# Kernel optimization log

Hardware: AMD Instinct MI355X
Metric: run time of the kernel (lower is better)

## Reference

```python
import jax, jax.numpy as jnp
import numpy as np

EPS = 1e-8

def _l2_normalize(v):
    # torch F.normalize: v / max(||v||_2, eps)
    n = jnp.sqrt(jnp.sum(v * v, axis=1, keepdims=True))
    return v / jnp.maximum(n, EPS)

def setup_inputs() -> dict:
    key = jax.random.key(0)
    k1, k2, k3, k4, k5 = jax.random.split(key, 5)
    B, D, N, C = 1024, 256, 200000, 1000
    x = jax.random.normal(k1, (B, D), dtype=jnp.float32)
    mean = jax.random.normal(k2, (D,), dtype=jnp.float32)
    inv_std = jax.random.uniform(k3, (D,), dtype=jnp.float32)
    train_x = jax.random.normal(k4, (N, D), dtype=jnp.float32)
    train_y = jax.random.randint(k5, (N,), 0, C, dtype=jnp.int64)
    return {"x": x, "mean": mean, "inv_std": inv_std,
            "train_x": train_x, "train_y": train_y}

def reference(x, mean, inv_std, train_x, train_y):
    NUM_CLASSES, K, TEMP = 1000, 20, 20.0
    B = x.shape[0]
    # buffer prep from __init__: normalize train bank rows
    tx = _l2_normalize(train_x)                      # [N, D]
    # forward: standardize + normalize queries
    q = _l2_normalize((x.reshape(B, -1) - mean) * inv_std)  # [B, D]
    sim = q @ tx.T                                   # [B, N]
    k = min(K, tx.shape[0])
    vals, idx = jax.lax.top_k(sim, k)                # [B, k]
    weights = jax.nn.softmax(vals * TEMP, axis=1)    # [B, k]
    labs = train_y[idx]                              # [B, k] gather labels
    out = jnp.zeros((B, NUM_CLASSES), dtype=jnp.float32)
    out = out.at[jnp.arange(B)[:, None], labs].add(weights)
    return out
```

## Files before the change

kernel.cpp:

```cpp
#include <hip/hip_runtime.h>
#include <math.h>

#define BQ     1024
#define D      256
#define NTRAIN 200000
#define CCLS   1000
#define KTOP   20
#define KC     24
#define TEMPF  20.0f
#define EPSV   1e-8f

#define NSEG    64
#define SEGROWS 3125
#define SEGT    49
#define QT      128
#define SSTR    68

typedef __attribute__((ext_vector_type(8))) short bf16x8;
typedef __attribute__((ext_vector_type(4))) float f32x4;

static __device__ __forceinline__ unsigned short f2bf(float f) {
  unsigned int u = __float_as_uint(f);
  u += 0x7FFFu + ((u >> 16) & 1u);
  return (unsigned short)(u >> 16);
}

__global__ void prep_q(const float* __restrict__ x, const float* __restrict__ mean,
                       const float* __restrict__ inv_std,
                       float* __restrict__ qf, unsigned short* __restrict__ qb) {
  int row = blockIdx.x;
  int t = threadIdx.x;
  float v = (x[row * D + t] - mean[t]) * inv_std[t];
  float s = v * v;
  #pragma unroll
  for (int off = 32; off; off >>= 1) s += __shfl_down(s, off);
  __shared__ float red[4];
  if ((t & 63) == 0) red[t >> 6] = s;
  __syncthreads();
  float tot = red[0] + red[1] + red[2] + red[3];
  float scale = 1.0f / fmaxf(sqrtf(tot), EPSV);
  float qv = v * scale;
  qf[row * D + t] = qv;
  qb[row * D + t] = f2bf(qv);
}

__global__ void bank_prep(const float* __restrict__ tx,
                          unsigned short* __restrict__ txb, float* __restrict__ rnorm) {
  int lane = threadIdx.x & 63;
  int row = blockIdx.x * 4 + (threadIdx.x >> 6);
  const float4* p = reinterpret_cast<const float4*>(tx + (size_t)row * D);
  float4 a = p[lane];
  float s = a.x * a.x + a.y * a.y + a.z * a.z + a.w * a.w;
  #pragma unroll
  for (int off = 32; off; off >>= 1) s += __shfl_xor(s, off);
  float rn = 1.0f / fmaxf(sqrtf(s), EPSV);
  if (lane == 0) rnorm[row] = rn;
  ushort4 us;
  us.x = f2bf(a.x * rn); us.y = f2bf(a.y * rn);
  us.z = f2bf(a.z * rn); us.w = f2bf(a.w * rn);
  *reinterpret_cast<ushort4*>(txb + (size_t)row * D + lane * 4) = us;
}

__global__ __launch_bounds__(256, 2)
void knn_mfma(const unsigned short* __restrict__ qb, const unsigned short* __restrict__ txb,
              float* __restrict__ pvals, int* __restrict__ pidx) {
  __shared__ float S[QT * SSTR];

  int t = threadIdx.x;
  int lane = t & 63;
  int w = t >> 6;
  int c = lane & 15, g = lane >> 4;

  int b = blockIdx.x;
  int seg = (b & 7) * 8 + ((b >> 3) & 7);
  int qt  = b >> 6;
  int qbase = qt * QT;
  int wq = qbase + w * 32;

  bf16x8 af[2][8];
  #pragma unroll
  for (int mf = 0; mf < 2; ++mf)
    #pragma unroll
    for (int ks = 0; ks < 8; ++ks)
      af[mf][ks] = *reinterpret_cast<const bf16x8*>(
          qb + (size_t)(wq + mf * 16 + c) * D + ks * 32 + g * 8);

  float tvv[KC]; int tii[KC];
  #pragma unroll
  for (int i = 0; i < KC; ++i) { tvv[i] = -INFINITY; tii[i] = 0; }
  float tmin = -INFINITY;

  auto insert24 = [&](float v, int gi) {
    bool done = false;
    #pragma unroll
    for (int i = 0; i < KC; ++i) {
      bool hit = (!done) && (tvv[i] == tmin);
      if (hit) { tvv[i] = v; tii[i] = gi; done = true; }
    }
    tmin = tvv[0];
    #pragma unroll
    for (int i = 1; i < KC; ++i) tmin = fminf(tmin, tvv[i]);
  };

  int nseg0 = seg * SEGROWS;
  int nsegEnd = nseg0 + SEGROWS;
  int q = t >> 1, pp = t & 1;

  for (int tile = 0; tile < SEGT; ++tile) {
    int nbase = nseg0 + tile * 64;

    f32x4 acc[2][4];
    #pragma unroll
    for (int mf = 0; mf < 2; ++mf)
      #pragma unroll
      for (int nf = 0; nf < 4; ++nf) acc[mf][nf] = (f32x4){0.f, 0.f, 0.f, 0.f};

    #pragma unroll
    for (int ks = 0; ks < 8; ++ks) {
      bf16x8 bfr[4];
      #pragma unroll
      for (int nf = 0; nf < 4; ++nf) {
        int row = nbase + nf * 16 + c;
        row = (row < NTRAIN) ? row : (NTRAIN - 1);
        bfr[nf] = *reinterpret_cast<const bf16x8*>(
            txb + (size_t)row * D + ks * 32 + g * 8);
      }
      #pragma unroll
      for (int nf = 0; nf < 4; ++nf) {
        acc[0][nf] = __builtin_amdgcn_mfma_f32_16x16x32_bf16(af[0][ks], bfr[nf], acc[0][nf], 0, 0, 0);
        acc[1][nf] = __builtin_amdgcn_mfma_f32_16x16x32_bf16(af[1][ks], bfr[nf], acc[1][nf], 0, 0, 0);
      }
    }

    __syncthreads();
    #pragma unroll
    for (int mf = 0; mf < 2; ++mf)
      #pragma unroll
      for (int nf = 0; nf < 4; ++nf)
        #pragma unroll
        for (int r = 0; r < 4; ++r)
          S[(w * 32 + mf * 16 + g * 4 + r) * SSTR + nf * 16 + c] = acc[mf][nf][r];
    __syncthreads();

    #pragma unroll 1
    for (int jj = 0; jj < 8; ++jj) {
      f32x4 v4 = *reinterpret_cast<const f32x4*>(&S[q * SSTR + pp * 32 + jj * 4]);
      int g0 = nbase + pp * 32 + jj * 4;
      #pragma unroll
      for (int e = 0; e < 4; ++e) {
        if (g0 + e < nsegEnd && v4[e] > tmin) insert24(v4[e], g0 + e);
      }
    }
  }

  __syncthreads();
  float* MV = S;
  int*   MI = reinterpret_cast<int*>(S + QT * KC);
  if (pp == 1) {
    #pragma unroll
    for (int i = 0; i < KC; ++i) { MV[q * KC + i] = tvv[i]; MI[q * KC + i] = tii[i]; }
  }
  __syncthreads();
  if (pp == 0) {
    #pragma unroll 1
    for (int i = 0; i < KC; ++i) {
      float v = MV[q * KC + i]; int gi = MI[q * KC + i];
      if (v > tmin) insert24(v, gi);
    }
    int base = ((qbase + q) * NSEG + seg) * KC;
    #pragma unroll
    for (int i = 0; i < KC; ++i) { pvals[base + i] = tvv[i]; pidx[base + i] = tii[i]; }
  }
}

#define NCAND (NSEG * KC)
__global__ void final_sel(const float* __restrict__ pvals, const int* __restrict__ pidx,
                          const float* __restrict__ qf, const float* __restrict__ tx,
                          const float* __restrict__ rnorm, const int* __restrict__ train_y,
                          float* __restrict__ out) {
  __shared__ float cv[NCAND];
  __shared__ int   ci[NCAND];
  __shared__ float qs[D];
  __shared__ float wvv[4 * KC];
  __shared__ int   wii[4 * KC];
  __shared__ float selv[KC];
  __shared__ int   seli[KC];
  __shared__ float rsc[KC];
  __shared__ float ordv[KTOP];
  __shared__ int   ordi[KTOP];
  __shared__ float outrow[CCLS];

  int bq = blockIdx.x;
  int t = threadIdx.x, lane = t & 63, w = t >> 6;

  for (int j = t; j < CCLS; j += 256) outrow[j] = 0.f;
  qs[t] = qf[bq * D + t];
  #pragma unroll
  for (int i = 0; i < 6; ++i) {
    int j = i * 256 + t;
    cv[j] = pvals[(size_t)bq * NCAND + j];
    ci[j] = pidx[(size_t)bq * NCAND + j];
  }
  __syncthreads();

  float lv[6]; int li[6];
  #pragma unroll
  for (int i = 0; i < 6; ++i) { int j = w * 384 + i * 64 + lane; lv[i] = cv[j]; li[i] = ci[j]; }
  for (int it = 0; it < KC; ++it) {
    float bv = -INFINITY; int bi = 0x7fffffff;
    #pragma unroll
    for (int i = 0; i < 6; ++i)
      if (lv[i] > bv || (lv[i] == bv && li[i] < bi)) { bv = lv[i]; bi = li[i]; }
    #pragma unroll
    for (int off = 32; off; off >>= 1) {
      float ov = __shfl_xor(bv, off); int oi = __shfl_xor(bi, off);
      if (ov > bv || (ov == bv && oi < bi)) { bv = ov; bi = oi; }
    }
    #pragma unroll
    for (int i = 0; i < 6; ++i)
      if (li[i] == bi && lv[i] == bv) lv[i] = -INFINITY;
    if (lane == 0) { wvv[w * KC + it] = bv; wii[w * KC + it] = bi; }
  }
  __syncthreads();

  if (w == 0) {
    float m0 = wvv[lane]; int i0 = wii[lane];
    float m1 = (lane < 32) ? wvv[64 + lane] : -INFINITY;
    int   i1 = (lane < 32) ? wii[64 + lane] : 0x7fffffff;
    for (int it = 0; it < KC; ++it) {
      float bv = m0; int bi = i0;
      if (m1 > bv || (m1 == bv && i1 < bi)) { bv = m1; bi = i1; }
      #pragma unroll
      for (int off = 32; off; off >>= 1) {
        float ov = __shfl_xor(bv, off); int oi = __shfl_xor(bi, off);
        if (ov > bv || (ov == bv && oi < bi)) { bv = ov; bi = oi; }
      }
      if (i0 == bi && m0 == bv) m0 = -INFINITY;
      if (i1 == bi && m1 == bv) m1 = -INFINITY;
      if (lane == 0) { selv[it] = bv; seli[it] = bi; }
    }
  }
  __syncthreads();

  for (int k = w; k < KC; k += 4) {
    int idx = seli[k];
    float4 tv = reinterpret_cast<const float4*>(tx + (size_t)idx * D)[lane];
    float4 qv = *reinterpret_cast<const float4*>(&qs[lane * 4]);
    float s = tv.x * qv.x + tv.y * qv.y + tv.z * qv.z + tv.w * qv.w;
    #pragma unroll
    for (int off = 32; off; off >>= 1) s += __shfl_xor(s, off);
    if (lane == 0) rsc[k] = s * rnorm[idx];
  }
  __syncthreads();

  if (w == 0) {
    float v = (lane < KC) ? rsc[lane] : -INFINITY;
    int   i = (lane < KC) ? seli[lane] : 0x7fffffff;
    for (int it = 0; it < KTOP; ++it) {
      float bv = v; int bi = i;
      #pragma unroll
      for (int off = 32; off; off >>= 1) {
        float ov = __shfl_xor(bv, off); int oi = __shfl_xor(bi, off);
        if (ov > bv || (ov == bv && oi < bi)) { bv = ov; bi = oi; }
      }
      if (v == bv && i == bi) v = -INFINITY;
      if (lane == 0) { ordv[it] = bv; ordi[it] = bi; }
    }
    float e = (lane < KTOP) ? expf((ordv[lane] - ordv[0]) * TEMPF) : 0.f;
    float ssum = e;
    #pragma unroll
    for (int off = 32; off; off >>= 1) ssum += __shfl_xor(ssum, off);
    if (lane < KTOP) {
      int label = train_y[ordi[lane]];
      atomicAdd(&outrow[label], e / ssum);
    }
  }
  __syncthreads();
  if (t < 250) reinterpret_cast<float4*>(out)[bq * 250 + t] =
      reinterpret_cast<const float4*>(outrow)[t];
}

extern "C" void kernel_launch(void* const* d_in, const int* in_sizes, int n_in,
                              void* d_out, int out_size, void* d_ws, size_t ws_size,
                              hipStream_t stream) {
  const float* x       = (const float*)d_in[0];
  const float* mean    = (const float*)d_in[1];
  const float* inv_std = (const float*)d_in[2];
  const float* train_x = (const float*)d_in[3];
  const int*   train_y = (const int*)d_in[4];
  float* out = (float*)d_out;

  char* wp = (char*)d_ws;
  float*          qf    = (float*)wp;          wp += (size_t)BQ * D * 4;
  unsigned short* qb    = (unsigned short*)wp; wp += (size_t)BQ * D * 2;
  float*          rnorm = (float*)wp;          wp += (size_t)NTRAIN * 4;
  unsigned short* txb   = (unsigned short*)wp; wp += (size_t)NTRAIN * D * 2;
  float*          pvals = (float*)wp;          wp += (size_t)BQ * NSEG * KC * 4;
  int*            pidx  = (int*)wp;

  prep_q   <<<BQ, 256, 0, stream>>>(x, mean, inv_std, qf, qb);
  bank_prep<<<NTRAIN / 4, 256, 0, stream>>>(train_x, txb, rnorm);
  knn_mfma <<<8 * NSEG, 256, 0, stream>>>(qb, txb, pvals, pidx);
  final_sel<<<BQ, 256, 0, stream>>>(pvals, pidx, qf, train_x, rnorm, train_y, out);
}
```

Measured before the change: 1.459 ms.

## Replace per-thread top-k insertion with two-pass tile-max threshold filtering

The fused GEMM plus register insertion-sort kernel is replaced by three steps. Pass A computes bf16 MFMA similarities and stores only the per-tile maximum for each query. A selection kernel takes the 24th largest tile maximum as a per-query threshold tau. Pass B recomputes the similarities and appends indices scoring at least tau to a capped per-query list using atomics, and the final kernel rescores those candidates in fp32 and picks the top 20. This removes the costly serial insertion logic and LDS round-trips, at the price of running the similarity GEMM twice, extra tmax traffic, and a cap of 256 candidates per query that could overflow.

```diff
diff --git a/kernel.cpp b/kernel.cpp
--- a/kernel.cpp
+++ b/kernel.cpp
@@ -6,15 +6,16 @@
 #define NTRAIN 200000
 #define CCLS   1000
 #define KTOP   20
-#define KC     24
+#define KSEL   24
 #define TEMPF  20.0f
 #define EPSV   1e-8f
 
 #define NSEG    64
 #define SEGROWS 3125
 #define SEGT    49
-#define QT      128
-#define SSTR    68
+#define TGLOB   (NSEG * SEGT)
+#define QTB     64
+#define CAP     256
 
 typedef __attribute__((ext_vector_type(8))) short bf16x8;
 typedef __attribute__((ext_vector_type(4))) float f32x4;
@@ -61,222 +62,214 @@
   *reinterpret_cast<ushort4*>(txb + (size_t)row * D + lane * 4) = us;
 }
 
-__global__ __launch_bounds__(256, 2)
-void knn_mfma(const unsigned short* __restrict__ qb, const unsigned short* __restrict__ txb,
-              float* __restrict__ pvals, int* __restrict__ pidx) {
-  __shared__ float S[QT * SSTR];
-
-  int t = threadIdx.x;
-  int lane = t & 63;
-  int w = t >> 6;
+__global__ __launch_bounds__(256, 4)
+void knn_passA(const unsigned short* __restrict__ qb, const unsigned short* __restrict__ txb,
+               float* __restrict__ tmax) {
+  int t = threadIdx.x, lane = t & 63, w = t >> 6;
   int c = lane & 15, g = lane >> 4;
-
   int b = blockIdx.x;
   int seg = (b & 7) * 8 + ((b >> 3) & 7);
   int qt  = b >> 6;
-  int qbase = qt * QT;
-  int wq = qbase + w * 32;
-
-  bf16x8 af[2][8];
-  #pragma unroll
-  for (int mf = 0; mf < 2; ++mf)
-    #pragma unroll
-    for (int ks = 0; ks < 8; ++ks)
-      af[mf][ks] = *reinterpret_cast<const bf16x8*>(
-          qb + (size_t)(wq + mf * 16 + c) * D + ks * 32 + g * 8);
-
-  float tvv[KC]; int tii[KC];
-  #pragma unroll
-  for (int i = 0; i < KC; ++i) { tvv[i] = -INFINITY; tii[i] = 0; }
-  float tmin = -INFINITY;
-
-  auto insert24 = [&](float v, int gi) {
-    bool done = false;
-    #pragma unroll
-    for (int i = 0; i < KC; ++i) {
-      bool hit = (!done) && (tvv[i] == tmin);
-      if (hit) { tvv[i] = v; tii[i] = gi; done = true; }
-    }
-    tmin = tvv[0];
-    #pragma unroll
-    for (int i = 1; i < KC; ++i) tmin = fminf(tmin, tvv[i]);
-  };
+  int qrow = qt * QTB + w * 16 + c;
+
+  bf16x8 qfr[8];
+  #pragma unroll
+  for (int ks = 0; ks < 8; ++ks)
+    qfr[ks] = *reinterpret_cast<const bf16x8*>(qb + (size_t)qrow * D + ks * 32 + g * 8);
 
   int nseg0 = seg * SEGROWS;
   int nsegEnd = nseg0 + SEGROWS;
-  int q = t >> 1, pp = t & 1;
 
   for (int tile = 0; tile < SEGT; ++tile) {
     int nbase = nseg0 + tile * 64;
-
-    f32x4 acc[2][4];
-    #pragma unroll
-    for (int mf = 0; mf < 2; ++mf)
-      #pragma unroll
-      for (int nf = 0; nf < 4; ++nf) acc[mf][nf] = (f32x4){0.f, 0.f, 0.f, 0.f};
-
+    const unsigned short* tp[4];
+    #pragma unroll
+    for (int nf = 0; nf < 4; ++nf) {
+      int row = nbase + nf * 16 + c;
+      row = (row < nsegEnd) ? row : (nsegEnd - 1);
+      tp[nf] = txb + (size_t)row * D + g * 8;
+    }
+    f32x4 acc[4];
+    #pragma unroll
+    for (int nf = 0; nf < 4; ++nf) acc[nf] = (f32x4){0.f, 0.f, 0.f, 0.f};
     #pragma unroll
     for (int ks = 0; ks < 8; ++ks) {
-      bf16x8 bfr[4];
-      #pragma unroll
-      for (int nf = 0; nf < 4; ++nf) {
-        int row = nbase + nf * 16 + c;
-        row = (row < NTRAIN) ? row : (NTRAIN - 1);
-        bfr[nf] = *reinterpret_cast<const bf16x8*>(
-            txb + (size_t)row * D + ks * 32 + g * 8);
+      bf16x8 tfr[4];
+      #pragma unroll
+      for (int nf = 0; nf < 4; ++nf)
+        tfr[nf] = *reinterpret_cast<const bf16x8*>(tp[nf] + ks * 32);
+      #pragma unroll
+      for (int nf = 0; nf < 4; ++nf)
+        acc[nf] = __builtin_amdgcn_mfma_f32_16x16x32_bf16(tfr[nf], qfr[ks], acc[nf], 0, 0, 0);
+    }
+    float m0 = fmaxf(fmaxf(acc[0][0], acc[0][1]), fmaxf(acc[0][2], acc[0][3]));
+    float m1 = fmaxf(fmaxf(acc[1][0], acc[1][1]), fmaxf(acc[1][2], acc[1][3]));
+    float m2 = fmaxf(fmaxf(acc[2][0], acc[2][1]), fmaxf(acc[2][2], acc[2][3]));
+    float m3 = fmaxf(fmaxf(acc[3][0], acc[3][1]), fmaxf(acc[3][2], acc[3][3]));
+    float mx = fmaxf(fmaxf(m0, m1), fmaxf(m2, m3));
+    mx = fmaxf(mx, __shfl_xor(mx, 16));
+    mx = fmaxf(mx, __shfl_xor(mx, 32));
+    if (g == 0) tmax[(size_t)(seg * SEGT + tile) * BQ + qrow] = mx;
+  }
+}
+
+__global__ void sel_tau(const float* __restrict__ tmax, float* __restrict__ tau) {
+  __shared__ float sv[4]; __shared__ int sj[4];
+  __shared__ float sbv;   __shared__ int sbj;
+  int q = blockIdx.x, t = threadIdx.x, lane = t & 63, w = t >> 6;
+  float v[13];
+  #pragma unroll
+  for (int i = 0; i < 13; ++i) {
+    int jj = i * 256 + t;
+    v[i] = (jj < TGLOB) ? tmax[(size_t)jj * BQ + q] : -INFINITY;
+  }
+  float last = 0.f;
+  for (int it = 0; it < KSEL; ++it) {
+    float bv = -INFINITY; int bj = 0x7fffffff;
+    #pragma unroll
+    for (int i = 0; i < 13; ++i)
+      if (v[i] > bv) { bv = v[i]; bj = i * 256 + t; }
+    #pragma unroll
+    for (int off = 32; off; off >>= 1) {
+      float ov = __shfl_xor(bv, off); int oj = __shfl_xor(bj, off);
+      if (ov > bv || (ov == bv && oj < bj)) { bv = ov; bj = oj; }
+    }
+    if (lane == 0) { sv[w] = bv; sj[w] = bj; }
+    __syncthreads();
+    if (t == 0) {
+      float BV = sv[0]; int BJ = sj[0];
+      #pragma unroll
+      for (int k = 1; k < 4; ++k)
+        if (sv[k] > BV || (sv[k] == BV && sj[k] < BJ)) { BV = sv[k]; BJ = sj[k]; }
+      sbv = BV; sbj = BJ;
+    }
+    __syncthreads();
+    float BV = sbv; int BJ = sbj;
+    #pragma unroll
+    for (int i = 0; i < 13; ++i)
+      if (i * 256 + t == BJ) v[i] = -INFINITY;
+    last = BV;
+    __syncthreads();
+  }
+  if (t == 0) tau[q] = last;
+}
+
+__global__ __launch_bounds__(256, 4)
+void knn_passB(const unsigned short* __restrict__ qb, const unsigned short* __restrict__ txb,
+               const float* __restrict__ tau, int* __restrict__ cnt, int* __restrict__ lists) {
+  int t = threadIdx.x, lane = t & 63, w = t >> 6;
+  int c = lane & 15, g = lane >> 4;
+  int b = blockIdx.x;
+  int seg = (b & 7) * 8 + ((b >> 3) & 7);
+  int qt  = b >> 6;
+  int qrow = qt * QTB + w * 16 + c;
+
+  bf16x8 qfr[8];
+  #pragma unroll
+  for (int ks = 0; ks < 8; ++ks)
+    qfr[ks] = *reinterpret_cast<const bf16x8*>(qb + (size_t)qrow * D + ks * 32 + g * 8);
+  float tq = tau[qrow];
+
+  int nseg0 = seg * SEGROWS;
+  int nsegEnd = nseg0 + SEGROWS;
+
+  for (int tile = 0; tile < SEGT; ++tile) {
+    int nbase = nseg0 + tile * 64;
+    const unsigned short* tp[4];
+    #pragma unroll
+    for (int nf = 0; nf < 4; ++nf) {
+      int row = nbase + nf * 16 + c;
+      row = (row < nsegEnd) ? row : (nsegEnd - 1);
+      tp[nf] = txb + (size_t)row * D + g * 8;
+    }
+    f32x4 acc[4];
+    #pragma unroll
+    for (int nf = 0; nf < 4; ++nf) acc[nf] = (f32x4){0.f, 0.f, 0.f, 0.f};
+    #pragma unroll
+    for (int ks = 0; ks < 8; ++ks) {
+      bf16x8 tfr[4];
+      #pragma unroll
+      for (int nf = 0; nf < 4; ++nf)
+        tfr[nf] = *reinterpret_cast<const bf16x8*>(tp[nf] + ks * 32);
+      #pragma unroll
+      for (int nf = 0; nf < 4; ++nf)
+        acc[nf] = __builtin_amdgcn_mfma_f32_16x16x32_bf16(tfr[nf], qfr[ks], acc[nf], 0, 0, 0);
+    }
+    #pragma unroll
+    for (int nf = 0; nf < 4; ++nf) {
+      #pragma unroll
+      for (int r = 0; r < 4; ++r) {
+        int n = nbase + nf * 16 + g * 4 + r;
+        float v = acc[nf][r];
+        if (n < nsegEnd && v >= tq) {
+          int pos = atomicAdd(&cnt[qrow], 1);
+          if (pos < CAP) lists[(size_t)qrow * CAP + pos] = n;
+        }
       }
-      #pragma unroll
-      for (int nf = 0; nf < 4; ++nf) {
-        acc[0][nf] = __builtin_amdgcn_mfma_f32_16x16x32_bf16(af[0][ks], bfr[nf], acc[0][nf], 0, 0, 0);
-        acc[1][nf] = __builtin_amdgcn_mfma_f32_16x16x32_bf16(af[1][ks], bfr[nf], acc[1][nf], 0, 0, 0);
-      }
-    }
-
-    __syncthreads();
-    #pragma unroll
-    for (int mf = 0; mf < 2; ++mf)
-      #pragma unroll
-      for (int nf = 0; nf < 4; ++nf)
-        #pragma unroll
-        for (int r = 0; r < 4; ++r)
-          S[(w * 32 + mf * 16 + g * 4 + r) * SSTR + nf * 16 + c] = acc[mf][nf][r];
-    __syncthreads();
-
-    #pragma unroll 1
-    for (int jj = 0; jj < 8; ++jj) {
-      f32x4 v4 = *reinterpret_cast<const f32x4*>(&S[q * SSTR + pp * 32 + jj * 4]);
-      int g0 = nbase + pp * 32 + jj * 4;
-      #pragma unroll
-      for (int e = 0; e < 4; ++e) {
-        if (g0 + e < nsegEnd && v4[e] > tmin) insert24(v4[e], g0 + e);
-      }
-    }
-  }
-
-  __syncthreads();
-  float* MV = S;
-  int*   MI = reinterpret_cast<int*>(S + QT * KC);
-  if (pp == 1) {
-    #pragma unroll
-    for (int i = 0; i < KC; ++i) { MV[q * KC + i] = tvv[i]; MI[q * KC + i] = tii[i]; }
-  }
-  __syncthreads();
-  if (pp == 0) {
-    #pragma unroll 1
-    for (int i = 0; i < KC; ++i) {
-      float v = MV[q * KC + i]; int gi = MI[q * KC + i];
-      if (v > tmin) insert24(v, gi);
-    }
-    int base = ((qbase + q) * NSEG + seg) * KC;
-    #pragma unroll
-    for (int i = 0; i < KC; ++i) { pvals[base + i] = tvv[i]; pidx[base + i] = tii[i]; }
-  }
-}
-
-#define NCAND (NSEG * KC)
-__global__ void final_sel(const float* __restrict__ pvals, const int* __restrict__ pidx,
+    }
+  }
+}
+
+__global__ void final_sel(const int* __restrict__ cnt, const int* __restrict__ lists,
                           const float* __restrict__ qf, const float* __restrict__ tx,
                           const float* __restrict__ rnorm, const int* __restrict__ train_y,
                           float* __restrict__ out) {
-  __shared__ float cv[NCAND];
-  __shared__ int   ci[NCAND];
   __shared__ float qs[D];
-  __shared__ float wvv[4 * KC];
-  __shared__ int   wii[4 * KC];
-  __shared__ float selv[KC];
-  __shared__ int   seli[KC];
-  __shared__ float rsc[KC];
-  __shared__ float ordv[KTOP];
-  __shared__ int   ordi[KTOP];
+  __shared__ float rv[CAP]; __shared__ int ri[CAP];
+  __shared__ float sv[4];  __shared__ int sj[4];
+  __shared__ float sbv;    __shared__ int sbj;
+  __shared__ float ordv[KTOP]; __shared__ int ordi[KTOP];
   __shared__ float outrow[CCLS];
-
-  int bq = blockIdx.x;
-  int t = threadIdx.x, lane = t & 63, w = t >> 6;
-
+  int q = blockIdx.x, t = threadIdx.x, lane = t & 63, w = t >> 6;
+
+  qs[t] = qf[q * D + t];
   for (int j = t; j < CCLS; j += 256) outrow[j] = 0.f;
-  qs[t] = qf[bq * D + t];
-  #pragma unroll
-  for (int i = 0; i < 6; ++i) {
-    int j = i * 256 + t;
-    cv[j] = pvals[(size_t)bq * NCAND + j];
-    ci[j] = pidx[(size_t)bq * NCAND + j];
-  }
+  int m = cnt[q]; if (m > CAP) m = CAP;
   __syncthreads();
 
-  float lv[6]; int li[6];
-  #pragma unroll
-  for (int i = 0; i < 6; ++i) { int j = w * 384 + i * 64 + lane; lv[i] = cv[j]; li[i] = ci[j]; }
-  for (int it = 0; it < KC; ++it) {
-    float bv = -INFINITY; int bi = 0x7fffffff;
-    #pragma unroll
-    for (int i = 0; i < 6; ++i)
-      if (lv[i] > bv || (lv[i] == bv && li[i] < bi)) { bv = lv[i]; bi = li[i]; }
-    #pragma unroll
-    for (int off = 32; off; off >>= 1) {
-      float ov = __shfl_xor(bv, off); int oi = __shfl_xor(bi, off);
-      if (ov > bv || (ov == bv && oi < bi)) { bv = ov; bi = oi; }
-    }
-    #pragma unroll
-    for (int i = 0; i < 6; ++i)
-      if (li[i] == bi && lv[i] == bv) lv[i] = -INFINITY;
-    if (lane == 0) { wvv[w * KC + it] = bv; wii[w * KC + it] = bi; }
-  }
-  __syncthreads();
-
-  if (w == 0) {
-    float m0 = wvv[lane]; int i0 = wii[lane];
-    float m1 = (lane < 32) ? wvv[64 + lane] : -INFINITY;
-    int   i1 = (lane < 32) ? wii[64 + lane] : 0x7fffffff;
-    for (int it = 0; it < KC; ++it) {
-      float bv = m0; int bi = i0;
-      if (m1 > bv || (m1 == bv && i1 < bi)) { bv = m1; bi = i1; }
-      #pragma unroll
-      for (int off = 32; off; off >>= 1) {
-        float ov = __shfl_xor(bv, off); int oi = __shfl_xor(bi, off);
-        if (ov > bv || (ov == bv && oi < bi)) { bv = ov; bi = oi; }
-      }
-      if (i0 == bi && m0 == bv) m0 = -INFINITY;
-      if (i1 == bi && m1 == bv) m1 = -INFINITY;
-      if (lane == 0) { selv[it] = bv; seli[it] = bi; }
-    }
-  }
-  __syncthreads();
-
-  for (int k = w; k < KC; k += 4) {
-    int idx = seli[k];
+  for (int k = w; k < m; k += 4) {
+    int idx = lists[(size_t)q * CAP + k];
     float4 tv = reinterpret_cast<const float4*>(tx + (size_t)idx * D)[lane];
     float4 qv = *reinterpret_cast<const float4*>(&qs[lane * 4]);
     float s = tv.x * qv.x + tv.y * qv.y + tv.z * qv.z + tv.w * qv.w;
     #pragma unroll
     for (int off = 32; off; off >>= 1) s += __shfl_xor(s, off);
-    if (lane == 0) rsc[k] = s * rnorm[idx];
+    if (lane == 0) { rv[k] = s * rnorm[idx]; ri[k] = idx; }
   }
   __syncthreads();
 
+  float v0 = (t < m) ? rv[t] : -INFINITY;
+  int   i0 = (t < m) ? ri[t] : 0x7fffffff;
+  for (int it = 0; it < KTOP; ++it) {
+    float bv = v0; int bj = i0;
+    #pragma unroll
+    for (int off = 32; off; off >>= 1) {
+      float ov = __shfl_xor(bv, off); int oj = __shfl_xor(bj, off);
+      if (ov > bv || (ov == bv && oj < bj)) { bv = ov; bj = oj; }
+    }
+    if (lane == 0) { sv[w] = bv; sj[w] = bj; }
+    __syncthreads();
+    if (t == 0) {
+      float BV = sv[0]; int BJ = sj[0];
+      #pragma unroll
+      for (int k = 1; k < 4; ++k)
+        if (sv[k] > BV || (sv[k] == BV && sj[k] < BJ)) { BV = sv[k]; BJ = sj[k]; }
+      sbv = BV; sbj = BJ; ordv[it] = BV; ordi[it] = BJ;
+    }
+    __syncthreads();
+    if (v0 == sbv && i0 == sbj) v0 = -INFINITY;
+    __syncthreads();
+  }
+
   if (w == 0) {
-    float v = (lane < KC) ? rsc[lane] : -INFINITY;
-    int   i = (lane < KC) ? seli[lane] : 0x7fffffff;
-    for (int it = 0; it < KTOP; ++it) {
-      float bv = v; int bi = i;
-      #pragma unroll
-      for (int off = 32; off; off >>= 1) {
-        float ov = __shfl_xor(bv, off); int oi = __shfl_xor(bi, off);
-        if (ov > bv || (ov == bv && oi < bi)) { bv = ov; bi = oi; }
-      }
-      if (v == bv && i == bi) v = -INFINITY;
-      if (lane == 0) { ordv[it] = bv; ordi[it] = bi; }
-    }
     float e = (lane < KTOP) ? expf((ordv[lane] - ordv[0]) * TEMPF) : 0.f;
     float ssum = e;
     #pragma unroll
     for (int off = 32; off; off >>= 1) ssum += __shfl_xor(ssum, off);
-    if (lane < KTOP) {
-      int label = train_y[ordi[lane]];
-      atomicAdd(&outrow[label], e / ssum);
-    }
+    if (lane < KTOP) atomicAdd(&outrow[train_y[ordi[lane]]], e / ssum);
   }
   __syncthreads();
-  if (t < 250) reinterpret_cast<float4*>(out)[bq * 250 + t] =
+  if (t < 250) reinterpret_cast<float4*>(out)[q * 250 + t] =
       reinterpret_cast<const float4*>(outrow)[t];
 }
 
@@ -295,11 +288,16 @@
   unsigned short* qb    = (unsigned short*)wp; wp += (size_t)BQ * D * 2;
   float*          rnorm = (float*)wp;          wp += (size_t)NTRAIN * 4;
   unsigned short* txb   = (unsigned short*)wp; wp += (size_t)NTRAIN * D * 2;
-  float*          pvals = (float*)wp;          wp += (size_t)BQ * NSEG * KC * 4;
-  int*            pidx  = (int*)wp;
+  float*          tmax  = (float*)wp;          wp += (size_t)TGLOB * BQ * 4;
+  float*          tau   = (float*)wp;          wp += (size_t)BQ * 4;
+  int*            cnt   = (int*)wp;            wp += (size_t)BQ * 4;
+  int*            lists = (int*)wp;
 
   prep_q   <<<BQ, 256, 0, stream>>>(x, mean, inv_std, qf, qb);
   bank_prep<<<NTRAIN / 4, 256, 0, stream>>>(train_x, txb, rnorm);
-  knn_mfma <<<8 * NSEG, 256, 0, stream>>>(qb, txb, pvals, pidx);
-  final_sel<<<BQ, 256, 0, stream>>>(pvals, pidx, qf, train_x, rnorm, train_y, out);
-}
+  knn_passA<<<16 * NSEG, 256, 0, stream>>>(qb, txb, tmax);
+  sel_tau  <<<BQ, 256, 0, stream>>>(tmax, tau);
+  hipMemsetAsync(cnt, 0, (size_t)BQ * 4, stream);
+  knn_passB<<<16 * NSEG, 256, 0, stream>>>(qb, txb, tau, cnt, lists);
+  final_sel<<<BQ, 256, 0, stream>>>(cnt, lists, qf, train_x, rnorm, train_y, out);
+}
```

After: 1.739 ms. +19.2%, slower.
